# Kernel tuning notes

Hardware: AMD Instinct MI355X
Metric: run time of the kernel (lower is better)

Reference implementation:

```python
import jax, jax.numpy as jnp
import numpy as np

T = 2048         # seq_len (nbatch in original code)
IN = 384         # input_size (npts)
H = 2 * IN       # hidden_dim = 768
NL = 10          # n_layers
NOUT = 384       # output_size


def setup_inputs() -> dict:
    key = jax.random.key(0)
    ks = jax.random.split(key, 12)
    s_in = 1.0 / np.sqrt(H)  # PyTorch GRU init scale
    inp = {
        "x": jax.random.normal(ks[0], (T, IN), dtype=jnp.float32),
        # layer 0 (input_size -> H)
        "w_ih0": jax.random.uniform(ks[1], (3 * H, IN), jnp.float32, -s_in, s_in),
        "w_hh0": jax.random.uniform(ks[2], (3 * H, H), jnp.float32, -s_in, s_in),
        "b_ih0": jax.random.uniform(ks[3], (3 * H,), jnp.float32, -s_in, s_in),
        "b_hh0": jax.random.uniform(ks[4], (3 * H,), jnp.float32, -s_in, s_in),
        # layers 1..9 (H -> H), stacked
        "w_ih": jax.random.uniform(ks[5], (NL - 1, 3 * H, H), jnp.float32, -s_in, s_in),
        "w_hh": jax.random.uniform(ks[6], (NL - 1, 3 * H, H), jnp.float32, -s_in, s_in),
        "b_ih": jax.random.uniform(ks[7], (NL - 1, 3 * H), jnp.float32, -s_in, s_in),
        "b_hh": jax.random.uniform(ks[8], (NL - 1, 3 * H), jnp.float32, -s_in, s_in),
        # final linear head
        "fc_w": jax.random.uniform(ks[9], (NOUT, H), jnp.float32, -s_in, s_in),
        "fc_b": jax.random.uniform(ks[10], (NOUT,), jnp.float32, -s_in, s_in),
    }
    return inp


def _gru_layer(xs, w_ih, w_hh, b_ih, b_hh):
    # xs: [T, D_in] -> ys: [T, H]. PyTorch GRU cell semantics.
    gi = xs @ w_ih.T + b_ih          # [T, 3H] input projections, batched GEMM up front

    def step(h, gi_t):
        gh = h @ w_hh.T + b_hh       # [3H]
        i_r, i_z, i_n = jnp.split(gi_t, 3)
        h_r, h_z, h_n = jnp.split(gh, 3)
        r = jax.nn.sigmoid(i_r + h_r)
        z = jax.nn.sigmoid(i_z + h_z)
        n = jnp.tanh(i_n + r * h_n)
        h_new = (1.0 - z) * n + z * h
        return h_new, h_new

    h0 = jnp.zeros((xs.shape[1] if False else w_hh.shape[1],), xs.dtype)  # [H]
    _, ys = jax.lax.scan(step, h0, gi)
    return ys


def reference(x, w_ih0, w_hh0, b_ih0, b_hh0, w_ih, w_hh, b_ih, b_hh, fc_w, fc_b):
    # batch_size = 1 in the original; hidden initialized to zeros each call.
    h = _gru_layer(x, w_ih0, w_hh0, b_ih0, b_hh0)   # layer 0
    for l in range(NL - 1):                           # layers 1..9 (fixed small loop)
        h = _gru_layer(h, w_ih[l], w_hh[l], b_ih[l], b_hh[l])
    out = h @ fc_w.T + fc_b                           # [T, NOUT]
    return out
```

## Files before the change

kernel.cpp:

```cpp
#include <hip/hip_runtime.h>


#define T_SEQ 2048
#define H_DIM 768
#define IN0   384
#define G3    2304
#define NLAYER 10
#define BPL   24
#define NBLK  (NLAYER * BPL)
#define UPB   32
#define NTHR  512
#define NOUT  384
#define CTR_STRIDE 32
#define RING  16
#define WIH_STRIDE 776
#define HCS_STRIDE 52
#define HSD_STRIDE 56
#define HSD0_STRIDE 32

typedef _Float16 half2_t __attribute__((ext_vector_type(2)));
typedef _Float16 half8_t __attribute__((ext_vector_type(8)));
typedef unsigned long long u64;

__device__ __forceinline__ float sigm(float x) { return 1.0f / (1.0f + __expf(-x)); }

__device__ __forceinline__ u64 ld64(const u64* p) {
    return __hip_atomic_load(p, __ATOMIC_RELAXED, __HIP_MEMORY_SCOPE_AGENT);
}
__device__ __forceinline__ void st64(u64* p, u64 v) {
    __hip_atomic_store(p, v, __ATOMIC_RELAXED, __HIP_MEMORY_SCOPE_AGENT);
}
__device__ __forceinline__ unsigned ldctr(const unsigned* p) {
    return __hip_atomic_load(p, __ATOMIC_RELAXED, __HIP_MEMORY_SCOPE_AGENT);
}
__device__ __forceinline__ unsigned tag_of(u64 u) { return (unsigned)(u >> 32); }
__device__ __forceinline__ float    val_of(u64 u) { return __uint_as_float((unsigned)u); }
__device__ __forceinline__ u64      pack(float v, unsigned t) {
    return ((u64)t << 32) | (u64)__float_as_uint(v);
}

__device__ __forceinline__ float dot8(half8_t h, half8_t w, float acc) {
    union U { half8_t v; unsigned u[4]; };
    U H; H.v = h; U W; W.v = w;
#pragma unroll
    for (int j = 0; j < 4; ++j) {
#if __has_builtin(__builtin_amdgcn_fdot2)
        acc = __builtin_amdgcn_fdot2(__builtin_bit_cast(half2_t, H.u[j]),
                                     __builtin_bit_cast(half2_t, W.u[j]), acc, false);
#else
        half2_t a = __builtin_bit_cast(half2_t, H.u[j]);
        half2_t b = __builtin_bit_cast(half2_t, W.u[j]);
        asm volatile("v_dot2_f32_f16 %0, %1, %2, %0" : "+v"(acc) : "v"(a), "v"(b));
#endif
    }
    return acc;
}

extern "C" __global__ __launch_bounds__(NTHR, 1) void gru_flow(
    const float* __restrict__ x,
    const float* __restrict__ wih0,
    const float* __restrict__ whh0,
    const float* __restrict__ bih0,
    const float* __restrict__ bhh0,
    const float* __restrict__ wihS,
    const float* __restrict__ whhS,
    const float* __restrict__ bihS,
    const float* __restrict__ bhhS,
    u64* __restrict__ ring64,
    float* __restrict__ h9,
    unsigned int* __restrict__ ctr)
{
    __shared__ __align__(16) _Float16 wih16[96 * WIH_STRIDE];
    __shared__ __align__(16) float    hcs[2][16 * HCS_STRIDE];
    __shared__ __align__(16) _Float16 hsd16[2][16 * HSD_STRIDE];

    const int tid  = threadIdx.x;
    const int lane = tid & 63;
    const int wv   = tid >> 6;
    const int p    = lane & 15;
    const int ulocal = wv * 4 + (lane >> 4);
    const int bid  = blockIdx.x;
    const int layer = bid / BPL;
    const int sub   = bid % BPL;
    const int uglob = sub * UPB + ulocal;
    const int Din   = layer ? H_DIM : IN0;
    const bool w2   = (tid < 256);

    const float* wihL = layer ? wihS + (size_t)(layer - 1) * G3 * H_DIM : wih0;
    const float* whhL = layer ? whhS + (size_t)(layer - 1) * G3 * H_DIM : whh0;
    const float* bihL = layer ? bihS + (size_t)(layer - 1) * G3 : bih0;
    const float* bhhL = layer ? bhhS + (size_t)(layer - 1) * G3 : bhh0;

    float4 wr[3][12];
#pragma unroll
    for (int gate = 0; gate < 3; ++gate) {
        const float4* src = (const float4*)(whhL + (size_t)(uglob + gate * H_DIM) * H_DIM + 48 * p);
#pragma unroll
        for (int i = 0; i < 12; ++i) wr[gate][i] = src[i];
    }
    const float bhr  = bhhL[uglob], bhz = bhhL[uglob + H_DIM], bhn  = bhhL[uglob + 2 * H_DIM];
    const float bir  = bihL[uglob], biz = bihL[uglob + H_DIM], bin_ = bihL[uglob + 2 * H_DIM];

    for (int rr = 0; rr < 12; ++rr) {
        const int r = wv * 12 + rr;
        const int u = r / 3, G = r % 3;
        const float* src = wihL + (size_t)(sub * UPB + u + G * H_DIM) * Din;
        _Float16* dst = wih16 + r * WIH_STRIDE;
        for (int k = lane; k < Din; k += 64) dst[k] = (_Float16)src[k];
    }
    __syncthreads();

    float gi_r = 0.f, gi_z = 0.f, gi_n = 0.f;
    auto ih_gemv = [&](int b) {
        float sr = 0.f, sz = 0.f, sn = 0.f;
        if (layer) {
            const half8_t* h8 = (const half8_t*)(&hsd16[b][p * HSD_STRIDE]);
            const half8_t* w0 = (const half8_t*)(wih16 + (ulocal * 3 + 0) * WIH_STRIDE + 48 * p);
            const half8_t* w1 = (const half8_t*)(wih16 + (ulocal * 3 + 1) * WIH_STRIDE + 48 * p);
            const half8_t* wn = (const half8_t*)(wih16 + (ulocal * 3 + 2) * WIH_STRIDE + 48 * p);
#pragma unroll
            for (int i = 0; i < 6; ++i) {
                const half8_t hv = h8[i];
                sr = dot8(hv, w0[i], sr);
                sz = dot8(hv, w1[i], sz);
                sn = dot8(hv, wn[i], sn);
            }
        } else {
            const half8_t* h8 = (const half8_t*)(&hsd16[b][p * HSD0_STRIDE]);
            const half8_t* w0 = (const half8_t*)(wih16 + (ulocal * 3 + 0) * WIH_STRIDE + 24 * p);
            const half8_t* w1 = (const half8_t*)(wih16 + (ulocal * 3 + 1) * WIH_STRIDE + 24 * p);
            const half8_t* wn = (const half8_t*)(wih16 + (ulocal * 3 + 2) * WIH_STRIDE + 24 * p);
#pragma unroll
            for (int i = 0; i < 3; ++i) {
                const half8_t hv = h8[i];
                sr = dot8(hv, w0[i], sr);
                sz = dot8(hv, w1[i], sz);
                sn = dot8(hv, wn[i], sn);
            }
        }
#pragma unroll
        for (int off = 1; off <= 8; off <<= 1) {
            sr += __shfl_xor(sr, off, 64);
            sz += __shfl_xor(sz, off, 64);
            sn += __shfl_xor(sn, off, 64);
        }
        gi_r = sr + bir; gi_z = sz + biz; gi_n = sn + bin_;
    };

    if (layer) {
        const u64* sp = ring64 + (size_t)(layer - 1) * RING * H_DIM;
        u64 a = ld64(sp + tid);
        while (tag_of(a) != 1u) a = ld64(sp + tid);
        hsd16[1][(tid / 48) * HSD_STRIDE + tid % 48] = (_Float16)val_of(a);
        if (w2) {
            u64 c = ld64(sp + tid + 512);
            while (tag_of(c) != 1u) c = ld64(sp + tid + 512);
            hsd16[1][((tid + 512) / 48) * HSD_STRIDE + (tid + 512) % 48] = (_Float16)val_of(c);
        }
    } else {
        if (tid < IN0) hsd16[1][(tid / 24) * HSD0_STRIDE + tid % 24] = (_Float16)x[tid];
    }
    __syncthreads();
    ih_gemv(1);

    u64 ca0 = 0, ca1 = 0, sa0 = 0, sa1 = 0;
    float xs = 0.f;
    if (layer) {
        const u64* sp = ring64 + ((size_t)(layer - 1) * RING + 1) * H_DIM;
        sa0 = ld64(sp + tid);
        if (w2) sa1 = ld64(sp + tid + 512);
    } else if (tid < IN0) {
        xs = x[IN0 + tid];
    }

    unsigned bp = 0;

    for (int t = 0; t < T_SEQ; ++t) {
        const int b = t & 1;
        const bool have_s = (t + 1) < T_SEQ;

        if (layer != NLAYER - 1 && t >= 16 && (t & 3) == 0) {
            const unsigned tgt = 24u * (unsigned)((t - 12) >> 2);
            while (bp < tgt) {
                __builtin_amdgcn_s_sleep(2);
                bp = ldctr(&ctr[(layer + 1) * CTR_STRIDE]);
            }
        }

        if (t > 0) {
            const u64* hr = ring64 + ((size_t)layer * RING + ((t - 1) & (RING - 1))) * H_DIM;
            while (tag_of(ca0) != (unsigned)t) ca0 = ld64(hr + tid);
            hcs[b][(tid / 48) * HCS_STRIDE + tid % 48] = val_of(ca0);
            if (w2) {
                while (tag_of(ca1) != (unsigned)t) ca1 = ld64(hr + tid + 512);
                hcs[b][((tid + 512) / 48) * HCS_STRIDE + (tid + 512) % 48] = val_of(ca1);
            }
        }

        if (have_s) {
            if (layer) {
                const u64* sp = ring64 + ((size_t)(layer - 1) * RING + ((t + 1) & (RING - 1))) * H_DIM;
                while (tag_of(sa0) != (unsigned)(t + 2)) sa0 = ld64(sp + tid);
                hsd16[b][(tid / 48) * HSD_STRIDE + tid % 48] = (_Float16)val_of(sa0);
                if (w2) {
                    while (tag_of(sa1) != (unsigned)(t + 2)) sa1 = ld64(sp + tid + 512);
                    hsd16[b][((tid + 512) / 48) * HSD_STRIDE + (tid + 512) % 48] = (_Float16)val_of(sa1);
                }
            } else {
                if (tid < IN0) hsd16[b][(tid / 24) * HSD0_STRIDE + tid % 24] = (_Float16)xs;
            }
        }

        __syncthreads();

        float ar = 0.f, az = 0.f, an = 0.f;
        if (t > 0) {
            const float4* hs = (const float4*)(&hcs[b][p * HCS_STRIDE]);
#pragma unroll
            for (int i = 0; i < 12; ++i) {
                const float4 h4 = hs[i];
                ar += h4.x * wr[0][i].x + h4.y * wr[0][i].y + h4.z * wr[0][i].z + h4.w * wr[0][i].w;
                az += h4.x * wr[1][i].x + h4.y * wr[1][i].y + h4.z * wr[1][i].z + h4.w * wr[1][i].w;
                an += h4.x * wr[2][i].x + h4.y * wr[2][i].y + h4.z * wr[2][i].z + h4.w * wr[2][i].w;
            }
        }
#pragma unroll
        for (int off = 1; off <= 8; off <<= 1) {
            ar += __shfl_xor(ar, off, 64);
            az += __shfl_xor(az, off, 64);
            an += __shfl_xor(an, off, 64);
        }
        if (p == 0) {
            const float hp = (t > 0) ? hcs[b][(uglob / 48) * HCS_STRIDE + uglob % 48] : 0.f;
            const float r = sigm(ar + bhr + gi_r);
            const float z = sigm(az + bhz + gi_z);
            const float n = tanhf(gi_n + r * (an + bhn));
            const float hnew = (1.f - z) * n + z * hp;
            st64(&ring64[((size_t)layer * RING + (t & (RING - 1))) * H_DIM + uglob],
                 pack(hnew, (unsigned)(t + 1)));
            if (layer == NLAYER - 1) h9[(size_t)t * H_DIM + uglob] = hnew;
        }

        if (have_s) {
            const u64* hrn = ring64 + ((size_t)layer * RING + (t & (RING - 1))) * H_DIM;
            ca0 = ld64(hrn + tid);
            if (w2) ca1 = ld64(hrn + tid + 512);
            if ((t + 2) < T_SEQ) {
                if (layer) {
                    const u64* spn = ring64 + ((size_t)(layer - 1) * RING + ((t + 2) & (RING - 1))) * H_DIM;
                    sa0 = ld64(spn + tid);
                    if (w2) sa1 = ld64(spn + tid + 512);
                } else if (tid < IN0) {
                    xs = x[(size_t)(t + 2) * IN0 + tid];
                }
            }
        }

        if (have_s) ih_gemv(b);

        if ((t & 3) == 3) {
            if (tid == 0 && layer)
                __hip_atomic_fetch_add(&ctr[layer * CTR_STRIDE], 1u,
                                       __ATOMIC_RELAXED, __HIP_MEMORY_SCOPE_AGENT);
            if (layer != NLAYER - 1)
                bp = ldctr(&ctr[(layer + 1) * CTR_STRIDE]);
        }
    }
}

extern "C" __global__ __launch_bounds__(NOUT, 1) void fc_head(
    const float* __restrict__ h,
    const float* __restrict__ fw,
    const float* __restrict__ fb,
    float* __restrict__ out)
{
    __shared__ float hs[H_DIM];
    const int t = blockIdx.x;
    const float* hr = h + (size_t)t * H_DIM;
    for (int k = threadIdx.x; k < H_DIM; k += NOUT) hs[k] = hr[k];
    __syncthreads();

    const int o = threadIdx.x;
    const float4* wr4 = (const float4*)(fw + (size_t)o * H_DIM);
    const float4* hs4 = (const float4*)hs;
    float acc = fb[o];
#pragma unroll 8
    for (int k = 0; k < H_DIM / 4; ++k) {
        const float4 w = wr4[k], hv = hs4[k];
        acc += w.x * hv.x + w.y * hv.y + w.z * hv.z + w.w * hv.w;
    }
    out[(size_t)t * NOUT + o] = acc;
}

extern "C" void kernel_launch(void* const* d_in, const int* in_sizes, int n_in,
                              void* d_out, int out_size, void* d_ws, size_t ws_size,
                              hipStream_t stream)
{
    const float* x    = (const float*)d_in[0];
    const float* wih0 = (const float*)d_in[1];
    const float* whh0 = (const float*)d_in[2];
    const float* bih0 = (const float*)d_in[3];
    const float* bhh0 = (const float*)d_in[4];
    const float* wihS = (const float*)d_in[5];
    const float* whhS = (const float*)d_in[6];
    const float* bihS = (const float*)d_in[7];
    const float* bhhS = (const float*)d_in[8];
    const float* fcw  = (const float*)d_in[9];
    const float* fcb  = (const float*)d_in[10];

    char* ws = (char*)d_ws;
    unsigned int* ctr = (unsigned int*)ws;
    u64* ring64 = (u64*)(ws + 65536);
    float* h9   = (float*)(ws + 65536 + (size_t)NLAYER * RING * H_DIM * 8);

    hipMemsetAsync(ctr, 0, 65536, stream);
    hipMemsetAsync(ring64, 0, (size_t)NLAYER * RING * H_DIM * 8, stream);

    hipLaunchKernelGGL(gru_flow, dim3(NBLK), dim3(NTHR), 0, stream,
                       x, wih0, whh0, bih0, bhh0, wihS, whhS, bihS, bhhS,
                       ring64, h9, ctr);

    hipLaunchKernelGGL(fc_head, dim3(T_SEQ), dim3(NOUT), 0, stream,
                       h9, fcw, fcb, (float*)d_out);
}
```

Measured before the change: 7.000 ms.

## Deepen input-projection lookahead to two steps and single-buffer shared staging

Layer-input staging and the input GEMV now run two timesteps ahead instead of one. This means the wait on the previous layer's ring slot targets an older step and puts more slack between layers. The double-buffered shared arrays become single buffers, which adds a second barrier per timestep. The hidden-state spin-wait keeps two loads in flight, and gate math now runs on all lanes, with only lane p==0 storing. The extra barrier per step may offset the gain from looser cross-layer coupling.

```diff
diff --git a/kernel.cpp b/kernel.cpp
--- a/kernel.cpp
+++ b/kernel.cpp
@@ -71,8 +71,8 @@
     unsigned int* __restrict__ ctr)
 {
     __shared__ __align__(16) _Float16 wih16[96 * WIH_STRIDE];
-    __shared__ __align__(16) float    hcs[2][16 * HCS_STRIDE];
-    __shared__ __align__(16) _Float16 hsd16[2][16 * HSD_STRIDE];
+    __shared__ __align__(16) float    hcs[16 * HCS_STRIDE];
+    __shared__ __align__(16) _Float16 hsd16[16 * HSD_STRIDE];
 
     const int tid  = threadIdx.x;
     const int lane = tid & 63;
@@ -110,11 +110,27 @@
     }
     __syncthreads();
 
-    float gi_r = 0.f, gi_z = 0.f, gi_n = 0.f;
-    auto ih_gemv = [&](int b) {
+    auto spin1 = [&](u64 cached, const u64* addr, unsigned tgt) -> u64 {
+        u64 v = cached;
+        while (tag_of(v) != tgt) v = ld64(addr);
+        return v;
+    };
+    auto spin2 = [&](u64 cached, const u64* addr, unsigned tgt) -> u64 {
+        u64 v = cached;
+        if (tag_of(v) == tgt) return v;
+        u64 v2 = ld64(addr);
+        for (;;) {
+            v = ld64(addr);
+            if (tag_of(v2) == tgt) return v2;
+            v2 = ld64(addr);
+            if (tag_of(v) == tgt) return v;
+        }
+    };
+
+    auto ih_gemv = [&](float& gr, float& gz, float& gn) {
         float sr = 0.f, sz = 0.f, sn = 0.f;
         if (layer) {
-            const half8_t* h8 = (const half8_t*)(&hsd16[b][p * HSD_STRIDE]);
+            const half8_t* h8 = (const half8_t*)(hsd16 + p * HSD_STRIDE);
             const half8_t* w0 = (const half8_t*)(wih16 + (ulocal * 3 + 0) * WIH_STRIDE + 48 * p);
             const half8_t* w1 = (const half8_t*)(wih16 + (ulocal * 3 + 1) * WIH_STRIDE + 48 * p);
             const half8_t* wn = (const half8_t*)(wih16 + (ulocal * 3 + 2) * WIH_STRIDE + 48 * p);
@@ -126,7 +142,7 @@
                 sn = dot8(hv, wn[i], sn);
             }
         } else {
-            const half8_t* h8 = (const half8_t*)(&hsd16[b][p * HSD0_STRIDE]);
+            const half8_t* h8 = (const half8_t*)(hsd16 + p * HSD0_STRIDE);
             const half8_t* w0 = (const half8_t*)(wih16 + (ulocal * 3 + 0) * WIH_STRIDE + 24 * p);
             const half8_t* w1 = (const half8_t*)(wih16 + (ulocal * 3 + 1) * WIH_STRIDE + 24 * p);
             const half8_t* wn = (const half8_t*)(wih16 + (ulocal * 3 + 2) * WIH_STRIDE + 24 * p);
@@ -144,41 +160,51 @@
             sz += __shfl_xor(sz, off, 64);
             sn += __shfl_xor(sn, off, 64);
         }
-        gi_r = sr + bir; gi_z = sz + biz; gi_n = sn + bin_;
+        gr = sr + bir; gz = sz + biz; gn = sn + bin_;
     };
 
+    auto stage_hsd = [&](const u64* sp, unsigned tgt) {
+        const u64 a = spin1(0, sp + tid, tgt);
+        hsd16[(tid / 48) * HSD_STRIDE + tid % 48] = (_Float16)val_of(a);
+        if (w2) {
+            const u64 c = spin1(0, sp + tid + 512, tgt);
+            hsd16[((tid + 512) / 48) * HSD_STRIDE + (tid + 512) % 48] = (_Float16)val_of(c);
+        }
+    };
+
+    float gA_r, gA_z, gA_n, gB_r, gB_z, gB_n;
     if (layer) {
-        const u64* sp = ring64 + (size_t)(layer - 1) * RING * H_DIM;
-        u64 a = ld64(sp + tid);
-        while (tag_of(a) != 1u) a = ld64(sp + tid);
-        hsd16[1][(tid / 48) * HSD_STRIDE + tid % 48] = (_Float16)val_of(a);
-        if (w2) {
-            u64 c = ld64(sp + tid + 512);
-            while (tag_of(c) != 1u) c = ld64(sp + tid + 512);
-            hsd16[1][((tid + 512) / 48) * HSD_STRIDE + (tid + 512) % 48] = (_Float16)val_of(c);
-        }
+        const u64* base = ring64 + (size_t)(layer - 1) * RING * H_DIM;
+        stage_hsd(base, 1u);
+        __syncthreads();
+        ih_gemv(gA_r, gA_z, gA_n);
+        __syncthreads();
+        stage_hsd(base + H_DIM, 2u);
+        __syncthreads();
+        ih_gemv(gB_r, gB_z, gB_n);
     } else {
-        if (tid < IN0) hsd16[1][(tid / 24) * HSD0_STRIDE + tid % 24] = (_Float16)x[tid];
-    }
-    __syncthreads();
-    ih_gemv(1);
+        if (tid < IN0) hsd16[(tid / 24) * HSD0_STRIDE + tid % 24] = (_Float16)x[tid];
+        __syncthreads();
+        ih_gemv(gA_r, gA_z, gA_n);
+        __syncthreads();
+        if (tid < IN0) hsd16[(tid / 24) * HSD0_STRIDE + tid % 24] = (_Float16)x[IN0 + tid];
+        __syncthreads();
+        ih_gemv(gB_r, gB_z, gB_n);
+    }
 
     u64 ca0 = 0, ca1 = 0, sa0 = 0, sa1 = 0;
     float xs = 0.f;
     if (layer) {
-        const u64* sp = ring64 + ((size_t)(layer - 1) * RING + 1) * H_DIM;
+        const u64* sp = ring64 + ((size_t)(layer - 1) * RING + 2) * H_DIM;
         sa0 = ld64(sp + tid);
         if (w2) sa1 = ld64(sp + tid + 512);
     } else if (tid < IN0) {
-        xs = x[IN0 + tid];
+        xs = x[2 * IN0 + tid];
     }
 
     unsigned bp = 0;
 
     for (int t = 0; t < T_SEQ; ++t) {
-        const int b = t & 1;
-        const bool have_s = (t + 1) < T_SEQ;
-
         if (layer != NLAYER - 1 && t >= 16 && (t & 3) == 0) {
             const unsigned tgt = 24u * (unsigned)((t - 12) >> 2);
             while (bp < tgt) {
@@ -189,25 +215,11 @@
 
         if (t > 0) {
             const u64* hr = ring64 + ((size_t)layer * RING + ((t - 1) & (RING - 1))) * H_DIM;
-            while (tag_of(ca0) != (unsigned)t) ca0 = ld64(hr + tid);
-            hcs[b][(tid / 48) * HCS_STRIDE + tid % 48] = val_of(ca0);
+            const u64 a = spin2(ca0, hr + tid, (unsigned)t);
+            hcs[(tid / 48) * HCS_STRIDE + tid % 48] = val_of(a);
             if (w2) {
-                while (tag_of(ca1) != (unsigned)t) ca1 = ld64(hr + tid + 512);
-                hcs[b][((tid + 512) / 48) * HCS_STRIDE + (tid + 512) % 48] = val_of(ca1);
-            }
-        }
-
-        if (have_s) {
-            if (layer) {
-                const u64* sp = ring64 + ((size_t)(layer - 1) * RING + ((t + 1) & (RING - 1))) * H_DIM;
-                while (tag_of(sa0) != (unsigned)(t + 2)) sa0 = ld64(sp + tid);
-                hsd16[b][(tid / 48) * HSD_STRIDE + tid % 48] = (_Float16)val_of(sa0);
-                if (w2) {
-                    while (tag_of(sa1) != (unsigned)(t + 2)) sa1 = ld64(sp + tid + 512);
-                    hsd16[b][((tid + 512) / 48) * HSD_STRIDE + (tid + 512) % 48] = (_Float16)val_of(sa1);
-                }
-            } else {
-                if (tid < IN0) hsd16[b][(tid / 24) * HSD0_STRIDE + tid % 24] = (_Float16)xs;
+                const u64 c = spin2(ca1, hr + tid + 512, (unsigned)t);
+                hcs[((tid + 512) / 48) * HCS_STRIDE + (tid + 512) % 48] = val_of(c);
             }
         }
 
@@ -215,7 +227,7 @@
 
         float ar = 0.f, az = 0.f, an = 0.f;
         if (t > 0) {
-            const float4* hs = (const float4*)(&hcs[b][p * HCS_STRIDE]);
+            const float4* hs = (const float4*)(hcs + p * HCS_STRIDE);
 #pragma unroll
             for (int i = 0; i < 12; ++i) {
                 const float4 h4 = hs[i];
@@ -230,33 +242,54 @@
             az += __shfl_xor(az, off, 64);
             an += __shfl_xor(an, off, 64);
         }
-        if (p == 0) {
-            const float hp = (t > 0) ? hcs[b][(uglob / 48) * HCS_STRIDE + uglob % 48] : 0.f;
-            const float r = sigm(ar + bhr + gi_r);
-            const float z = sigm(az + bhz + gi_z);
-            const float n = tanhf(gi_n + r * (an + bhn));
+        {
+            const float hp = (t > 0) ? hcs[(uglob / 48) * HCS_STRIDE + uglob % 48] : 0.f;
+            const float r = sigm(ar + bhr + gA_r);
+            const float z = sigm(az + bhz + gA_z);
+            const float n = tanhf(gA_n + r * (an + bhn));
             const float hnew = (1.f - z) * n + z * hp;
-            st64(&ring64[((size_t)layer * RING + (t & (RING - 1))) * H_DIM + uglob],
-                 pack(hnew, (unsigned)(t + 1)));
-            if (layer == NLAYER - 1) h9[(size_t)t * H_DIM + uglob] = hnew;
-        }
-
-        if (have_s) {
+            if (p == 0) {
+                st64(&ring64[((size_t)layer * RING + (t & (RING - 1))) * H_DIM + uglob],
+                     pack(hnew, (unsigned)(t + 1)));
+                if (layer == NLAYER - 1) h9[(size_t)t * H_DIM + uglob] = hnew;
+            }
+        }
+
+        if ((t + 1) < T_SEQ) {
             const u64* hrn = ring64 + ((size_t)layer * RING + (t & (RING - 1))) * H_DIM;
             ca0 = ld64(hrn + tid);
             if (w2) ca1 = ld64(hrn + tid + 512);
-            if ((t + 2) < T_SEQ) {
+            if ((t + 3) < T_SEQ) {
                 if (layer) {
-                    const u64* spn = ring64 + ((size_t)(layer - 1) * RING + ((t + 2) & (RING - 1))) * H_DIM;
+                    const u64* spn = ring64 + ((size_t)(layer - 1) * RING + ((t + 3) & (RING - 1))) * H_DIM;
                     sa0 = ld64(spn + tid);
                     if (w2) sa1 = ld64(spn + tid + 512);
                 } else if (tid < IN0) {
-                    xs = x[(size_t)(t + 2) * IN0 + tid];
+                    xs = x[(size_t)(t + 3) * IN0 + tid];
                 }
             }
         }
 
-        if (have_s) ih_gemv(b);
+        if ((t + 2) < T_SEQ) {
+            if (layer) {
+                const u64* sp = ring64 + ((size_t)(layer - 1) * RING + ((t + 2) & (RING - 1))) * H_DIM;
+                const u64 a = spin1(sa0, sp + tid, (unsigned)(t + 3));
+                hsd16[(tid / 48) * HSD_STRIDE + tid % 48] = (_Float16)val_of(a);
+                if (w2) {
+                    const u64 c = spin1(sa1, sp + tid + 512, (unsigned)(t + 3));
+                    hsd16[((tid + 512) / 48) * HSD_STRIDE + (tid + 512) % 48] = (_Float16)val_of(c);
+                }
+            } else {
+                if (tid < IN0) hsd16[(tid / 24) * HSD0_STRIDE + tid % 24] = (_Float16)xs;
+            }
+            __syncthreads();
+            float gn_r, gn_z, gn_n;
+            ih_gemv(gn_r, gn_z, gn_n);
+            gA_r = gB_r; gA_z = gB_z; gA_n = gB_n;
+            gB_r = gn_r; gB_z = gn_z; gB_n = gn_n;
+        } else {
+            gA_r = gB_r; gA_z = gB_z; gA_n = gB_n;
+        }
 
         if ((t & 3) == 3) {
             if (tid == 0 && layer)
```

New measurement: 7.576 ms. +8.2%, slower.

## Pack two hidden values per 64-bit ring slot using low-mantissa-bit tags

Applied to the files above, without the earlier changes.

Changes the inter-block ring-buffer format so that each 64-bit slot carries two fp32 hidden values. A 5-bit step tag is embedded in the low mantissa bits of each value, replacing the earlier layout of one value plus a 32-bit tag. This halves the ring traffic and the number of polling loads: 384 threads each load one word instead of 768 loads spread across 512 threads. Producers pair adjacent units with a shuffle before storing. The cost is that the 5 stolen mantissa bits truncate the propagated hidden state, and the tag wraps at 32, which depends on the ring depth and back-pressure keeping producers within that window.

```diff
diff --git a/kernel.cpp b/kernel.cpp
--- a/kernel.cpp
+++ b/kernel.cpp
@@ -13,6 +13,7 @@
 #define NOUT  384
 #define CTR_STRIDE 32
 #define RING  16
+#define WPR   384
 #define WIH_STRIDE 776
 #define HCS_STRIDE 52
 #define HSD_STRIDE 56
@@ -33,10 +34,8 @@
 __device__ __forceinline__ unsigned ldctr(const unsigned* p) {
     return __hip_atomic_load(p, __ATOMIC_RELAXED, __HIP_MEMORY_SCOPE_AGENT);
 }
-__device__ __forceinline__ unsigned tag_of(u64 u) { return (unsigned)(u >> 32); }
-__device__ __forceinline__ float    val_of(u64 u) { return __uint_as_float((unsigned)u); }
-__device__ __forceinline__ u64      pack(float v, unsigned t) {
-    return ((u64)t << 32) | (u64)__float_as_uint(v);
+__device__ __forceinline__ int tagok(u64 v, unsigned tg) {
+    return (((unsigned)v & 31u) == tg) & ((((unsigned)(v >> 32)) & 31u) == tg);
 }
 
 __device__ __forceinline__ float dot8(half8_t h, half8_t w, float acc) {
@@ -84,7 +83,6 @@
     const int sub   = bid % BPL;
     const int uglob = sub * UPB + ulocal;
     const int Din   = layer ? H_DIM : IN0;
-    const bool w2   = (tid < 256);
 
     const float* wihL = layer ? wihS + (size_t)(layer - 1) * G3 * H_DIM : wih0;
     const float* whhL = layer ? whhS + (size_t)(layer - 1) * G3 * H_DIM : whh0;
@@ -109,6 +107,15 @@
         for (int k = lane; k < Din; k += 64) dst[k] = (_Float16)src[k];
     }
     __syncthreads();
+
+    auto stage_hsd = [&](int b, int w, u64 v) {
+        const int s = w / 24, idx = (2 * w) % 48;
+        const _Float16 a = (_Float16)__uint_as_float((unsigned)v & ~31u);
+        const _Float16 c = (_Float16)__uint_as_float((unsigned)(v >> 32) & ~31u);
+        const unsigned pk = (unsigned)__builtin_bit_cast(unsigned short, a)
+                          | ((unsigned)__builtin_bit_cast(unsigned short, c) << 16);
+        *(unsigned*)&hsd16[b][s * HSD_STRIDE + idx] = pk;
+    };
 
     float gi_r = 0.f, gi_z = 0.f, gi_n = 0.f;
     auto ih_gemv = [&](int b) {
@@ -148,14 +155,11 @@
     };
 
     if (layer) {
-        const u64* sp = ring64 + (size_t)(layer - 1) * RING * H_DIM;
-        u64 a = ld64(sp + tid);
-        while (tag_of(a) != 1u) a = ld64(sp + tid);
-        hsd16[1][(tid / 48) * HSD_STRIDE + tid % 48] = (_Float16)val_of(a);
-        if (w2) {
-            u64 c = ld64(sp + tid + 512);
-            while (tag_of(c) != 1u) c = ld64(sp + tid + 512);
-            hsd16[1][((tid + 512) / 48) * HSD_STRIDE + (tid + 512) % 48] = (_Float16)val_of(c);
+        if (tid < WPR) {
+            const u64* sp = ring64 + (size_t)(layer - 1) * RING * WPR;
+            u64 v = 0;
+            while (!tagok(v, 1u)) v = ld64(sp + tid);
+            stage_hsd(1, tid, v);
         }
     } else {
         if (tid < IN0) hsd16[1][(tid / 24) * HSD0_STRIDE + tid % 24] = (_Float16)x[tid];
@@ -163,14 +167,11 @@
     __syncthreads();
     ih_gemv(1);
 
-    u64 ca0 = 0, ca1 = 0, sa0 = 0, sa1 = 0;
+    u64 ca0 = 0, sa0 = 0;
     float xs = 0.f;
-    if (layer) {
-        const u64* sp = ring64 + ((size_t)(layer - 1) * RING + 1) * H_DIM;
-        sa0 = ld64(sp + tid);
-        if (w2) sa1 = ld64(sp + tid + 512);
-    } else if (tid < IN0) {
-        xs = x[IN0 + tid];
+    if (tid < WPR) {
+        if (layer) sa0 = ld64(ring64 + ((size_t)(layer - 1) * RING + 1) * WPR + tid);
+        else       xs  = x[IN0 + tid];
     }
 
     unsigned bp = 0;
@@ -187,24 +188,26 @@
             }
         }
 
-        if (t > 0) {
-            const u64* hr = ring64 + ((size_t)layer * RING + ((t - 1) & (RING - 1))) * H_DIM;
-            while (tag_of(ca0) != (unsigned)t) ca0 = ld64(hr + tid);
-            hcs[b][(tid / 48) * HCS_STRIDE + tid % 48] = val_of(ca0);
-            if (w2) {
-                while (tag_of(ca1) != (unsigned)t) ca1 = ld64(hr + tid + 512);
-                hcs[b][((tid + 512) / 48) * HCS_STRIDE + (tid + 512) % 48] = val_of(ca1);
-            }
+        if (t > 0 && tid < WPR) {
+            const u64* hr = ring64 + ((size_t)layer * RING + ((t - 1) & (RING - 1))) * WPR;
+            const unsigned tg = (unsigned)t & 31u;
+            u64 v = ca0;
+            while (!tagok(v, tg)) v = ld64(hr + tid);
+            const int s = tid / 24, idx = (2 * tid) % 48;
+            float2 hv;
+            hv.x = __uint_as_float((unsigned)v & ~31u);
+            hv.y = __uint_as_float((unsigned)(v >> 32) & ~31u);
+            *(float2*)&hcs[b][s * HCS_STRIDE + idx] = hv;
         }
 
         if (have_s) {
             if (layer) {
-                const u64* sp = ring64 + ((size_t)(layer - 1) * RING + ((t + 1) & (RING - 1))) * H_DIM;
-                while (tag_of(sa0) != (unsigned)(t + 2)) sa0 = ld64(sp + tid);
-                hsd16[b][(tid / 48) * HSD_STRIDE + tid % 48] = (_Float16)val_of(sa0);
-                if (w2) {
-                    while (tag_of(sa1) != (unsigned)(t + 2)) sa1 = ld64(sp + tid + 512);
-                    hsd16[b][((tid + 512) / 48) * HSD_STRIDE + (tid + 512) % 48] = (_Float16)val_of(sa1);
+                if (tid < WPR) {
+                    const u64* sp = ring64 + ((size_t)(layer - 1) * RING + ((t + 1) & (RING - 1))) * WPR;
+                    const unsigned tg2 = (unsigned)(t + 2) & 31u;
+                    u64 v = sa0;
+                    while (!tagok(v, tg2)) v = ld64(sp + tid);
+                    stage_hsd(b, tid, v);
                 }
             } else {
                 if (tid < IN0) hsd16[b][(tid / 24) * HSD0_STRIDE + tid % 24] = (_Float16)xs;
@@ -230,29 +233,28 @@
             az += __shfl_xor(az, off, 64);
             an += __shfl_xor(an, off, 64);
         }
-        if (p == 0) {
+        {
             const float hp = (t > 0) ? hcs[b][(uglob / 48) * HCS_STRIDE + uglob % 48] : 0.f;
             const float r = sigm(ar + bhr + gi_r);
             const float z = sigm(az + bhz + gi_z);
             const float n = tanhf(gi_n + r * (an + bhn));
             const float hnew = (1.f - z) * n + z * hp;
-            st64(&ring64[((size_t)layer * RING + (t & (RING - 1))) * H_DIM + uglob],
-                 pack(hnew, (unsigned)(t + 1)));
-            if (layer == NLAYER - 1) h9[(size_t)t * H_DIM + uglob] = hnew;
-        }
-
-        if (have_s) {
-            const u64* hrn = ring64 + ((size_t)layer * RING + (t & (RING - 1))) * H_DIM;
-            ca0 = ld64(hrn + tid);
-            if (w2) ca1 = ld64(hrn + tid + 512);
+            const float hpart = __shfl_xor(hnew, 16, 64);
+            if (p == 0 && (lane & 16) == 0) {
+                const unsigned tg1 = (unsigned)(t + 1) & 31u;
+                const unsigned lo = (__float_as_uint(hnew)  & ~31u) | tg1;
+                const unsigned hi = (__float_as_uint(hpart) & ~31u) | tg1;
+                st64(&ring64[((size_t)layer * RING + (t & (RING - 1))) * WPR + (uglob >> 1)],
+                     ((u64)hi << 32) | (u64)lo);
+            }
+            if (layer == NLAYER - 1 && p == 0) h9[(size_t)t * H_DIM + uglob] = hnew;
+        }
+
+        if (have_s && tid < WPR) {
+            ca0 = ld64(ring64 + ((size_t)layer * RING + (t & (RING - 1))) * WPR + tid);
             if ((t + 2) < T_SEQ) {
-                if (layer) {
-                    const u64* spn = ring64 + ((size_t)(layer - 1) * RING + ((t + 2) & (RING - 1))) * H_DIM;
-                    sa0 = ld64(spn + tid);
-                    if (w2) sa1 = ld64(spn + tid + 512);
-                } else if (tid < IN0) {
-                    xs = x[(size_t)(t + 2) * IN0 + tid];
-                }
+                if (layer) sa0 = ld64(ring64 + ((size_t)(layer - 1) * RING + ((t + 2) & (RING - 1))) * WPR + tid);
+                else       xs  = x[(size_t)(t + 2) * IN0 + tid];
             }
         }
 
@@ -311,10 +313,10 @@
     char* ws = (char*)d_ws;
     unsigned int* ctr = (unsigned int*)ws;
     u64* ring64 = (u64*)(ws + 65536);
-    float* h9   = (float*)(ws + 65536 + (size_t)NLAYER * RING * H_DIM * 8);
+    float* h9   = (float*)(ws + 65536 + (size_t)NLAYER * RING * WPR * 8);
 
     hipMemsetAsync(ctr, 0, 65536, stream);
-    hipMemsetAsync(ring64, 0, (size_t)NLAYER * RING * H_DIM * 8, stream);
+    hipMemsetAsync(ring64, 0, (size_t)NLAYER * RING * WPR * 8, stream);
 
     hipLaunchKernelGGL(gru_flow, dim3(NBLK), dim3(NTHR), 0, stream,
                        x, wih0, whh0, bih0, bhh0, wihS, whhS, bihS, bhhS,
```

After: 7.046 ms. Within noise of the previous version (+0.7%).
